# Kernel tuning notes

Measured on AMD Instinct MI355X. Metric: run time of the kernel, lower is better.

Reference implementation:

```python
import jax, jax.numpy as jnp
import numpy as np
import math

B, S, D = 1, 512, 512
N = 8
DH = D // N  # 64


def setup_inputs() -> dict:
    key = jax.random.key(0)
    ks = jax.random.split(key, 12)
    s = 1.0 / math.sqrt(D)
    return {
        "hidden_states": jax.random.normal(ks[0], (B, S, D), dtype=jnp.float32),
        "attention_mask": jnp.ones((B, S), dtype=jnp.float32),
        # Linear weights stored as [in, out] (math-equivalent to torch x @ W.T + b)
        "Wq": jax.random.normal(ks[1], (D, D), dtype=jnp.float32) * s,
        "bq": jax.random.normal(ks[2], (D,), dtype=jnp.float32) * 0.01,
        "Wk": jax.random.normal(ks[3], (D, D), dtype=jnp.float32) * s,
        "bk": jax.random.normal(ks[4], (D,), dtype=jnp.float32) * 0.01,
        "Wv": jax.random.normal(ks[5], (D, D), dtype=jnp.float32) * s,
        "bv": jax.random.normal(ks[6], (D,), dtype=jnp.float32) * 0.01,
        "Wo": jax.random.normal(ks[7], (D, D), dtype=jnp.float32) * s,
        "bo": jax.random.normal(ks[8], (D,), dtype=jnp.float32) * 0.01,
        "gamma": jnp.ones((1,), dtype=jnp.float32) * math.sqrt(DH),
        "alpha": jnp.zeros((1,), dtype=jnp.float32),
    }


def _heads(x):
    # [B,S,D] -> [B,N,S,DH]
    return x.reshape(B, S, N, DH).transpose(0, 2, 1, 3)


def reference(hidden_states, attention_mask, Wq, bq, Wk, bk, Wv, bv, Wo, bo, gamma, alpha):
    q = _heads(hidden_states @ Wq + bq)  # [B,N,S,DH]
    k = _heads(hidden_states @ Wk + bk)
    v = _heads(hidden_states @ Wv + bv)

    # Manhattan-distance scores: z[b,n,i,j] = sum_d |q - k|
    abs_diff = jnp.abs(q[:, :, :, None, :] - k[:, :, None, :, :])  # [B,N,S,S,DH]
    z = abs_diff.sum(-1) / (gamma * math.sqrt(DH))  # [B,N,S,S]
    z_prime = jax.nn.relu(z - alpha)

    # mask: [B,S] -> [B,1,1,S]; masked-out keys get huge inhibition
    z_prime = z_prime + (1.0 - attention_mask)[:, None, None, :] * 1e10

    # inhibition: context[b,n,i,d] = sum_j relu(v[b,n,j,d] - z'[b,n,i,j])
    inhibited = jax.nn.relu(v[:, :, None, :, :] - z_prime[..., None])  # [B,N,S,S,DH]
    context = inhibited.sum(axis=3)  # [B,N,S,DH]  (dropout is identity at eval)

    context = context.transpose(0, 2, 1, 3).reshape(B, S, D)
    return context @ Wo + bo
```

## Files before the change

### kernel.cpp

```cpp
#include <hip/hip_runtime.h>

#define S 512
#define Dm 512

typedef __bf16 bf16x8 __attribute__((ext_vector_type(8)));
typedef float f32x4 __attribute__((ext_vector_type(4)));

template<bool A_BF16, bool TRANSQK>
__global__ __launch_bounds__(256) void gemm_icvt(
    const void* __restrict__ Aptr,
    const float* __restrict__ W0, const float* __restrict__ W1, const float* __restrict__ W2,
    const float* __restrict__ b0, const float* __restrict__ b1, const float* __restrict__ b2,
    float* __restrict__ O0, float* __restrict__ O1, float* __restrict__ O2)
{
    int blk = blockIdx.x;
    int m = blk >> 8;
    int tile = blk & 255;
    const float* W = (m == 0) ? W0 : (m == 1) ? W1 : W2;
    const float* bias = (m == 0) ? b0 : (m == 1) ? b1 : b2;
    float* O = (m == 0) ? O0 : (m == 1) ? O1 : O2;
    int rt = tile >> 4, ct = tile & 15;

    int u = threadIdx.x;
    int w = u >> 6, lane = u & 63;
    int r = lane & 15, kg = lane >> 4;

    int row0 = (rt << 5) + ((w >> 1) << 4);
    int col0 = (ct << 5) + ((w & 1) << 4);

    const float* Bp = W + (kg << 3) * Dm + col0 + r;

    f32x4 acc = {0.f, 0.f, 0.f, 0.f};

    #pragma unroll 4
    for (int k0 = 0; k0 < Dm; k0 += 32) {
        bf16x8 a;
        if constexpr (A_BF16) {
            const __bf16* Ab = (const __bf16*)Aptr;
            a = *(const bf16x8*)(Ab + (row0 + r) * Dm + k0 + (kg << 3));
        } else {
            const float* Af = (const float*)Aptr;
            float4 a0 = *(const float4*)(Af + (row0 + r) * Dm + k0 + (kg << 3));
            float4 a1 = *(const float4*)(Af + (row0 + r) * Dm + k0 + (kg << 3) + 4);
            a[0] = (__bf16)a0.x; a[1] = (__bf16)a0.y; a[2] = (__bf16)a0.z; a[3] = (__bf16)a0.w;
            a[4] = (__bf16)a1.x; a[5] = (__bf16)a1.y; a[6] = (__bf16)a1.z; a[7] = (__bf16)a1.w;
        }
        bf16x8 b;
        #pragma unroll
        for (int t = 0; t < 8; ++t)
            b[t] = (__bf16)Bp[(k0 + t) * Dm];
        acc = __builtin_amdgcn_mfma_f32_16x16x32_bf16(a, b, acc, 0, 0, 0);
    }

    int orow = row0 + (kg << 2);
    float bb = bias[col0 + r];

    if constexpr (TRANSQK) {
        if (m < 2) {
            float4 o = make_float4(acc[0] + bb, acc[1] + bb, acc[2] + bb, acc[3] + bb);
            *(float4*)(O + (col0 + r) * S + orow) = o;
            return;
        }
    }
    #pragma unroll
    for (int t = 0; t < 4; ++t)
        O[(orow + t) * Dm + col0 + r] = acc[t] + bb;
}

__global__ __launch_bounds__(512) void zT_kernel(
    const float* __restrict__ QT, const float* __restrict__ KT,
    const float* __restrict__ mask, const float* __restrict__ gamma,
    const float* __restrict__ alpha,
    float* __restrict__ zp, float* __restrict__ Zpart)
{
    int blk = blockIdx.x;
    int h  = blk >> 6;
    int it = blk & 63;
    int i0 = it << 3;
    int c0 = h << 6;

    int u = threadIdx.x;
    int w = u >> 6, lane = u & 63;
    int jj = (w << 6) + lane;

    const float* kcol = KT + (c0 * S) + jj;
    const float* qrow = QT + (c0 * S) + i0;

    float acc[8] = {};
    #pragma unroll 4
    for (int d = 0; d < 64; ++d) {
        float kv = kcol[d * S];
        float4 qa = *(const float4*)(qrow + d * S);
        float4 qb = *(const float4*)(qrow + d * S + 4);
        acc[0] += fabsf(qa.x - kv);
        acc[1] += fabsf(qa.y - kv);
        acc[2] += fabsf(qa.z - kv);
        acc[3] += fabsf(qa.w - kv);
        acc[4] += fabsf(qb.x - kv);
        acc[5] += fabsf(qb.y - kv);
        acc[6] += fabsf(qb.z - kv);
        acc[7] += fabsf(qb.w - kv);
    }

    float sc = 1.0f / (gamma[0] * 8.0f);
    float al = alpha[0];
    float madd = (1.0f - mask[jj]) * 1e6f;

    float zpv[8];
    #pragma unroll
    for (int r = 0; r < 8; ++r) {
        zpv[r] = fmaxf(acc[r] * sc - al, 0.0f) + madd;
        zp[((h << 9) + i0 + r) * S + jj] = zpv[r];
    }

    #pragma unroll
    for (int r = 0; r < 8; ++r) {
        float v = zpv[r];
        v += __shfl_xor(v, 1, 64);
        v += __shfl_xor(v, 2, 64);
        v += __shfl_xor(v, 4, 64);
        v += __shfl_xor(v, 8, 64);
        v += __shfl_xor(v, 16, 64);
        v += __shfl_xor(v, 32, 64);
        zpv[r] = v;
    }
    if (lane == 0) {
        #pragma unroll
        for (int r = 0; r < 8; ++r)
            Zpart[((h << 9) + i0 + r) * 8 + w] = zpv[r];
    }
}

__global__ __launch_bounds__(512) void ctx_kernel(
    const float* __restrict__ V, const float* __restrict__ zp,
    const float* __restrict__ Zpart, __bf16* __restrict__ ctxb)
{
    int blk = blockIdx.x;
    int h = blk >> 6;
    int it = blk & 63;
    int i0 = it << 3;
    int c0 = h << 6;
    int u = threadIdx.x;
    int w = u >> 6, lane = u & 63;

    __shared__ float part[8][8][64];

    int wu = __builtin_amdgcn_readfirstlane(w);
    float acc[8][4] = {};

    #pragma unroll
    for (int cch = 0; cch < 4; ++cch) {
        int jg = (cch << 7) + (wu << 4);
        float vv[16];
        #pragma unroll
        for (int t = 0; t < 16; ++t)
            vv[t] = V[(jg + t) * Dm + c0 + lane];

        const float* zbase = zp + ((h << 9) + i0) * S + jg;
        #pragma unroll
        for (int ii = 0; ii < 8; ++ii) {
            const float* zrow = zbase + ii * S;
            #pragma unroll
            for (int q4 = 0; q4 < 4; ++q4) {
                float4 z4 = *(const float4*)(zrow + (q4 << 2));
                acc[ii][0] += fmaxf(vv[(q4 << 2) + 0], z4.x);
                acc[ii][1] += fmaxf(vv[(q4 << 2) + 1], z4.y);
                acc[ii][2] += fmaxf(vv[(q4 << 2) + 2], z4.z);
                acc[ii][3] += fmaxf(vv[(q4 << 2) + 3], z4.w);
            }
        }
    }

    #pragma unroll
    for (int ii = 0; ii < 8; ++ii)
        part[w][ii][lane] = (acc[ii][0] + acc[ii][1]) + (acc[ii][2] + acc[ii][3]);
    __syncthreads();
    {
        int ii = u >> 6;
        float s = 0.f;
        #pragma unroll
        for (int ww = 0; ww < 8; ++ww) s += part[ww][ii][lane];
        float zsum = 0.f;
        const float* zpr = Zpart + ((h << 9) + (i0 + ii)) * 8;
        #pragma unroll
        for (int p = 0; p < 8; ++p) zsum += zpr[p];
        ctxb[(i0 + ii) * Dm + c0 + lane] = (__bf16)(s - zsum);
    }
}

extern "C" void kernel_launch(void* const* d_in, const int* in_sizes, int n_in,
                              void* d_out, int out_size, void* d_ws, size_t ws_size,
                              hipStream_t stream) {
    const float* hs    = (const float*)d_in[0];
    const float* mask  = (const float*)d_in[1];
    const float* Wq    = (const float*)d_in[2];
    const float* bq    = (const float*)d_in[3];
    const float* Wk    = (const float*)d_in[4];
    const float* bk    = (const float*)d_in[5];
    const float* Wv    = (const float*)d_in[6];
    const float* bv    = (const float*)d_in[7];
    const float* Wo    = (const float*)d_in[8];
    const float* bo    = (const float*)d_in[9];
    const float* gamma = (const float*)d_in[10];
    const float* alpha = (const float*)d_in[11];
    float* out = (float*)d_out;

    char* base = (char*)d_ws;
    float*  zp    = (float*)(base);
    float*  Zpart = (float*)(base + (8u << 20));
    float*  QT    = (float*)(base + (8u << 20) + (128u << 10));
    float*  KT    = QT + S * Dm;
    float*  Vb    = KT + S * Dm;
    __bf16* Cbf   = (__bf16*)(Vb + S * Dm);

    hipLaunchKernelGGL((gemm_icvt<false, true>), dim3(768), dim3(256), 0, stream,
                       (const void*)hs, Wq, Wk, Wv, bq, bk, bv, QT, KT, Vb);
    hipLaunchKernelGGL(zT_kernel, dim3(512), dim3(512), 0, stream,
                       QT, KT, mask, gamma, alpha, zp, Zpart);
    hipLaunchKernelGGL(ctx_kernel, dim3(512), dim3(512), 0, stream,
                       Vb, zp, Zpart, Cbf);
    hipLaunchKernelGGL((gemm_icvt<true, false>), dim3(256), dim3(256), 0, stream,
                       (const void*)Cbf, Wo, Wo, Wo, bo, bo, bo, out, out, out);
}
```

Measured before the change: 56.83 us.

## Fuse score and context kernels via LDS; pre-transpose weights to bf16

Merges the Manhattan-score kernel and the inhibition-context kernel into one kernel. The 8x512 score tile stays in shared memory instead of going through an 8 MB global buffer, and the row sums are kept in LDS. Adds a prep kernel that converts hidden states to bf16 and transposes all four weight matrices to bf16 [out,in] layout. The GEMMs can then use contiguous 16-byte loads instead of strided scalar fp32 loads. The cost is an extra launch and extra transpose traffic on every call, plus 16 KB+ of LDS per block, which may reduce occupancy in the fused kernel.

Result: faster. 54.19 us (-4.6%).

```diff
diff --git a/kernel.cpp b/kernel.cpp
--- a/kernel.cpp
+++ b/kernel.cpp
@@ -6,17 +6,68 @@
 typedef __bf16 bf16x8 __attribute__((ext_vector_type(8)));
 typedef float f32x4 __attribute__((ext_vector_type(4)));
 
-template<bool A_BF16, bool TRANSQK>
-__global__ __launch_bounds__(256) void gemm_icvt(
-    const void* __restrict__ Aptr,
-    const float* __restrict__ W0, const float* __restrict__ W1, const float* __restrict__ W2,
+__global__ __launch_bounds__(256) void prep_kernel(
+    const float* __restrict__ hs,
+    const float* __restrict__ W0, const float* __restrict__ W1,
+    const float* __restrict__ W2, const float* __restrict__ W3,
+    __bf16* __restrict__ Abf,
+    __bf16* __restrict__ T0, __bf16* __restrict__ T1,
+    __bf16* __restrict__ T2, __bf16* __restrict__ T3)
+{
+    __shared__ __bf16 Tl[64][72];
+    int u = threadIdx.x;
+    if (blockIdx.x < 128) {
+        int i = (blockIdx.x * 256 + u) * 8;
+        float4 x0 = *(const float4*)(hs + i);
+        float4 x1 = *(const float4*)(hs + i + 4);
+        bf16x8 y;
+        y[0] = (__bf16)x0.x; y[1] = (__bf16)x0.y; y[2] = (__bf16)x0.z; y[3] = (__bf16)x0.w;
+        y[4] = (__bf16)x1.x; y[5] = (__bf16)x1.y; y[6] = (__bf16)x1.z; y[7] = (__bf16)x1.w;
+        *(bf16x8*)(Abf + i) = y;
+        return;
+    }
+    int blk = blockIdx.x - 128;
+    int m = blk >> 6;
+    int t = blk & 63;
+    const float* W = (m == 0) ? W0 : (m == 1) ? W1 : (m == 2) ? W2 : W3;
+    __bf16* T = (m == 0) ? T0 : (m == 1) ? T1 : (m == 2) ? T2 : T3;
+    int k0 = (t >> 3) << 6;
+    int n0 = (t & 7) << 6;
+    {
+        int kk = u >> 4;
+        int n4 = (u & 15) << 2;
+        #pragma unroll
+        for (int p = 0; p < 4; ++p) {
+            int k = kk + (p << 4);
+            float4 wv = *(const float4*)(W + (k0 + k) * Dm + n0 + n4);
+            Tl[n4 + 0][k] = (__bf16)wv.x;
+            Tl[n4 + 1][k] = (__bf16)wv.y;
+            Tl[n4 + 2][k] = (__bf16)wv.z;
+            Tl[n4 + 3][k] = (__bf16)wv.w;
+        }
+    }
+    __syncthreads();
+    {
+        int n = u >> 2;
+        int ks = (u & 3) << 4;
+        uint4 d0 = *(const uint4*)&Tl[n][ks];
+        uint4 d1 = *(const uint4*)&Tl[n][ks + 8];
+        *(uint4*)(T + (n0 + n) * Dm + k0 + ks) = d0;
+        *(uint4*)(T + (n0 + n) * Dm + k0 + ks + 8) = d1;
+    }
+}
+
+template<bool TRANSQK>
+__global__ __launch_bounds__(256) void gemm_bf(
+    const __bf16* __restrict__ Abf,
+    const __bf16* __restrict__ T0, const __bf16* __restrict__ T1, const __bf16* __restrict__ T2,
     const float* __restrict__ b0, const float* __restrict__ b1, const float* __restrict__ b2,
     float* __restrict__ O0, float* __restrict__ O1, float* __restrict__ O2)
 {
     int blk = blockIdx.x;
     int m = blk >> 8;
     int tile = blk & 255;
-    const float* W = (m == 0) ? W0 : (m == 1) ? W1 : W2;
+    const __bf16* T = (m == 0) ? T0 : (m == 1) ? T1 : T2;
     const float* bias = (m == 0) ? b0 : (m == 1) ? b1 : b2;
     float* O = (m == 0) ? O0 : (m == 1) ? O1 : O2;
     int rt = tile >> 4, ct = tile & 15;
@@ -28,27 +79,15 @@
     int row0 = (rt << 5) + ((w >> 1) << 4);
     int col0 = (ct << 5) + ((w & 1) << 4);
 
-    const float* Bp = W + (kg << 3) * Dm + col0 + r;
+    const __bf16* Ap = Abf + (row0 + r) * Dm + (kg << 3);
+    const __bf16* Bp = T + (col0 + r) * Dm + (kg << 3);
 
     f32x4 acc = {0.f, 0.f, 0.f, 0.f};
 
     #pragma unroll 4
     for (int k0 = 0; k0 < Dm; k0 += 32) {
-        bf16x8 a;
-        if constexpr (A_BF16) {
-            const __bf16* Ab = (const __bf16*)Aptr;
-            a = *(const bf16x8*)(Ab + (row0 + r) * Dm + k0 + (kg << 3));
-        } else {
-            const float* Af = (const float*)Aptr;
-            float4 a0 = *(const float4*)(Af + (row0 + r) * Dm + k0 + (kg << 3));
-            float4 a1 = *(const float4*)(Af + (row0 + r) * Dm + k0 + (kg << 3) + 4);
-            a[0] = (__bf16)a0.x; a[1] = (__bf16)a0.y; a[2] = (__bf16)a0.z; a[3] = (__bf16)a0.w;
-            a[4] = (__bf16)a1.x; a[5] = (__bf16)a1.y; a[6] = (__bf16)a1.z; a[7] = (__bf16)a1.w;
-        }
-        bf16x8 b;
-        #pragma unroll
-        for (int t = 0; t < 8; ++t)
-            b[t] = (__bf16)Bp[(k0 + t) * Dm];
+        bf16x8 a = *(const bf16x8*)(Ap + k0);
+        bf16x8 b = *(const bf16x8*)(Bp + k0);
         acc = __builtin_amdgcn_mfma_f32_16x16x32_bf16(a, b, acc, 0, 0, 0);
     }
 
@@ -67,11 +106,10 @@
         O[(orow + t) * Dm + col0 + r] = acc[t] + bb;
 }
 
-__global__ __launch_bounds__(512) void zT_kernel(
-    const float* __restrict__ QT, const float* __restrict__ KT,
+__global__ __launch_bounds__(512) void zctx_kernel(
+    const float* __restrict__ QT, const float* __restrict__ KT, const float* __restrict__ V,
     const float* __restrict__ mask, const float* __restrict__ gamma,
-    const float* __restrict__ alpha,
-    float* __restrict__ zp, float* __restrict__ Zpart)
+    const float* __restrict__ alpha, __bf16* __restrict__ ctxb)
 {
     int blk = blockIdx.x;
     int h  = blk >> 6;
@@ -82,6 +120,10 @@
     int u = threadIdx.x;
     int w = u >> 6, lane = u & 63;
     int jj = (w << 6) + lane;
+
+    __shared__ float zs[8][512];
+    __shared__ float zpart[8][8];
+    __shared__ float part[8][8][64];
 
     const float* kcol = KT + (c0 * S) + jj;
     const float* qrow = QT + (c0 * S) + i0;
@@ -110,7 +152,7 @@
     #pragma unroll
     for (int r = 0; r < 8; ++r) {
         zpv[r] = fmaxf(acc[r] * sc - al, 0.0f) + madd;
-        zp[((h << 9) + i0 + r) * S + jj] = zpv[r];
+        zs[r][jj] = zpv[r];
     }
 
     #pragma unroll
@@ -126,27 +168,12 @@
     }
     if (lane == 0) {
         #pragma unroll
-        for (int r = 0; r < 8; ++r)
-            Zpart[((h << 9) + i0 + r) * 8 + w] = zpv[r];
-    }
-}
-
-__global__ __launch_bounds__(512) void ctx_kernel(
-    const float* __restrict__ V, const float* __restrict__ zp,
-    const float* __restrict__ Zpart, __bf16* __restrict__ ctxb)
-{
-    int blk = blockIdx.x;
-    int h = blk >> 6;
-    int it = blk & 63;
-    int i0 = it << 3;
-    int c0 = h << 6;
-    int u = threadIdx.x;
-    int w = u >> 6, lane = u & 63;
-
-    __shared__ float part[8][8][64];
+        for (int r = 0; r < 8; ++r) zpart[w][r] = zpv[r];
+    }
+    __syncthreads();
 
     int wu = __builtin_amdgcn_readfirstlane(w);
-    float acc[8][4] = {};
+    float a2[8][4] = {};
 
     #pragma unroll
     for (int cch = 0; cch < 4; ++cch) {
@@ -156,34 +183,32 @@
         for (int t = 0; t < 16; ++t)
             vv[t] = V[(jg + t) * Dm + c0 + lane];
 
-        const float* zbase = zp + ((h << 9) + i0) * S + jg;
         #pragma unroll
         for (int ii = 0; ii < 8; ++ii) {
-            const float* zrow = zbase + ii * S;
             #pragma unroll
             for (int q4 = 0; q4 < 4; ++q4) {
-                float4 z4 = *(const float4*)(zrow + (q4 << 2));
-                acc[ii][0] += fmaxf(vv[(q4 << 2) + 0], z4.x);
-                acc[ii][1] += fmaxf(vv[(q4 << 2) + 1], z4.y);
-                acc[ii][2] += fmaxf(vv[(q4 << 2) + 2], z4.z);
-                acc[ii][3] += fmaxf(vv[(q4 << 2) + 3], z4.w);
+                float4 z4 = *(const float4*)&zs[ii][jg + (q4 << 2)];
+                a2[ii][0] += fmaxf(vv[(q4 << 2) + 0], z4.x);
+                a2[ii][1] += fmaxf(vv[(q4 << 2) + 1], z4.y);
+                a2[ii][2] += fmaxf(vv[(q4 << 2) + 2], z4.z);
+                a2[ii][3] += fmaxf(vv[(q4 << 2) + 3], z4.w);
             }
         }
     }
 
     #pragma unroll
     for (int ii = 0; ii < 8; ++ii)
-        part[w][ii][lane] = (acc[ii][0] + acc[ii][1]) + (acc[ii][2] + acc[ii][3]);
+        part[w][ii][lane] = (a2[ii][0] + a2[ii][1]) + (a2[ii][2] + a2[ii][3]);
     __syncthreads();
+
     {
         int ii = u >> 6;
         float s = 0.f;
         #pragma unroll
         for (int ww = 0; ww < 8; ++ww) s += part[ww][ii][lane];
         float zsum = 0.f;
-        const float* zpr = Zpart + ((h << 9) + (i0 + ii)) * 8;
-        #pragma unroll
-        for (int p = 0; p < 8; ++p) zsum += zpr[p];
+        #pragma unroll
+        for (int p = 0; p < 8; ++p) zsum += zpart[p][ii];
         ctxb[(i0 + ii) * Dm + c0 + lane] = (__bf16)(s - zsum);
     }
 }
@@ -206,19 +231,22 @@
     float* out = (float*)d_out;
 
     char* base = (char*)d_ws;
-    float*  zp    = (float*)(base);
-    float*  Zpart = (float*)(base + (8u << 20));
-    float*  QT    = (float*)(base + (8u << 20) + (128u << 10));
-    float*  KT    = QT + S * Dm;
-    float*  Vb    = KT + S * Dm;
-    __bf16* Cbf   = (__bf16*)(Vb + S * Dm);
-
-    hipLaunchKernelGGL((gemm_icvt<false, true>), dim3(768), dim3(256), 0, stream,
-                       (const void*)hs, Wq, Wk, Wv, bq, bk, bv, QT, KT, Vb);
-    hipLaunchKernelGGL(zT_kernel, dim3(512), dim3(512), 0, stream,
-                       QT, KT, mask, gamma, alpha, zp, Zpart);
-    hipLaunchKernelGGL(ctx_kernel, dim3(512), dim3(512), 0, stream,
-                       Vb, zp, Zpart, Cbf);
-    hipLaunchKernelGGL((gemm_icvt<true, false>), dim3(256), dim3(256), 0, stream,
-                       (const void*)Cbf, Wo, Wo, Wo, bo, bo, bo, out, out, out);
-}
+    float*  QT  = (float*)(base);
+    float*  KT  = QT + S * Dm;
+    float*  Vb  = KT + S * Dm;
+    __bf16* Abf = (__bf16*)(Vb + S * Dm);
+    __bf16* T0  = Abf + S * Dm;
+    __bf16* T1  = T0 + S * Dm;
+    __bf16* T2  = T1 + S * Dm;
+    __bf16* T3  = T2 + S * Dm;
+    __bf16* Cbf = T3 + S * Dm;
+
+    hipLaunchKernelGGL(prep_kernel, dim3(384), dim3(256), 0, stream,
+                       hs, Wq, Wk, Wv, Wo, Abf, T0, T1, T2, T3);
+    hipLaunchKernelGGL((gemm_bf<true>), dim3(768), dim3(256), 0, stream,
+                       Abf, T0, T1, T2, bq, bk, bv, QT, KT, Vb);
+    hipLaunchKernelGGL(zctx_kernel, dim3(512), dim3(512), 0, stream,
+                       QT, KT, Vb, mask, gamma, alpha, Cbf);
+    hipLaunchKernelGGL((gemm_bf<false>), dim3(256), dim3(256), 0, stream,
+                       Cbf, T3, T3, T3, bo, bo, bo, out, out, out);
+}
```

## Fuse score and context kernels via LDS; stage weight tiles through shared memory

Applied to the files above, without the earlier changes.

The Manhattan-score kernel and the inhibition-context kernel are merged. The 8x512 z' tile and the per-row partial sums now stay in LDS, so the 8 MB zp buffer no longer round-trips through global memory and one launch is dropped. The GEMM also stages the weight tile through LDS with coalesced float4 loads and a transposed bf16 layout, replacing strided per-element global loads. In exchange, both kernels use more LDS and extra barriers, which may lower occupancy.

Measured after the change: 56.01 us. About the same (-1.4%).

```diff
diff --git a/kernel.cpp b/kernel.cpp
--- a/kernel.cpp
+++ b/kernel.cpp
@@ -7,7 +7,7 @@
 typedef float f32x4 __attribute__((ext_vector_type(4)));
 
 template<bool A_BF16, bool TRANSQK>
-__global__ __launch_bounds__(256) void gemm_icvt(
+__global__ __launch_bounds__(256) void gemm_stage(
     const void* __restrict__ Aptr,
     const float* __restrict__ W0, const float* __restrict__ W1, const float* __restrict__ W2,
     const float* __restrict__ b0, const float* __restrict__ b1, const float* __restrict__ b2,
@@ -26,30 +26,50 @@
     int r = lane & 15, kg = lane >> 4;
 
     int row0 = (rt << 5) + ((w >> 1) << 4);
-    int col0 = (ct << 5) + ((w & 1) << 4);
-
-    const float* Bp = W + (kg << 3) * Dm + col0 + r;
+    int colb = ct << 5;
+    int col0 = colb + ((w & 1) << 4);
+
+    __shared__ __bf16 Tl[32][72];
 
     f32x4 acc = {0.f, 0.f, 0.f, 0.f};
 
-    #pragma unroll 4
-    for (int k0 = 0; k0 < Dm; k0 += 32) {
-        bf16x8 a;
-        if constexpr (A_BF16) {
-            const __bf16* Ab = (const __bf16*)Aptr;
-            a = *(const bf16x8*)(Ab + (row0 + r) * Dm + k0 + (kg << 3));
-        } else {
-            const float* Af = (const float*)Aptr;
-            float4 a0 = *(const float4*)(Af + (row0 + r) * Dm + k0 + (kg << 3));
-            float4 a1 = *(const float4*)(Af + (row0 + r) * Dm + k0 + (kg << 3) + 4);
-            a[0] = (__bf16)a0.x; a[1] = (__bf16)a0.y; a[2] = (__bf16)a0.z; a[3] = (__bf16)a0.w;
-            a[4] = (__bf16)a1.x; a[5] = (__bf16)a1.y; a[6] = (__bf16)a1.z; a[7] = (__bf16)a1.w;
-        }
-        bf16x8 b;
-        #pragma unroll
-        for (int t = 0; t < 8; ++t)
-            b[t] = (__bf16)Bp[(k0 + t) * Dm];
-        acc = __builtin_amdgcn_mfma_f32_16x16x32_bf16(a, b, acc, 0, 0, 0);
+    int skk = u >> 2;
+    int sn4 = (u & 3) << 3;
+
+    for (int k0 = 0; k0 < Dm; k0 += 64) {
+        {
+            const float* wp = W + (k0 + skk) * Dm + colb + sn4;
+            float4 w0v = *(const float4*)(wp);
+            float4 w1v = *(const float4*)(wp + 4);
+            Tl[sn4 + 0][skk] = (__bf16)w0v.x;
+            Tl[sn4 + 1][skk] = (__bf16)w0v.y;
+            Tl[sn4 + 2][skk] = (__bf16)w0v.z;
+            Tl[sn4 + 3][skk] = (__bf16)w0v.w;
+            Tl[sn4 + 4][skk] = (__bf16)w1v.x;
+            Tl[sn4 + 5][skk] = (__bf16)w1v.y;
+            Tl[sn4 + 6][skk] = (__bf16)w1v.z;
+            Tl[sn4 + 7][skk] = (__bf16)w1v.w;
+        }
+        __syncthreads();
+
+        #pragma unroll
+        for (int s = 0; s < 2; ++s) {
+            int ks = k0 + (s << 5);
+            bf16x8 a;
+            if constexpr (A_BF16) {
+                const __bf16* Ab = (const __bf16*)Aptr;
+                a = *(const bf16x8*)(Ab + (row0 + r) * Dm + ks + (kg << 3));
+            } else {
+                const float* Af = (const float*)Aptr;
+                float4 a0 = *(const float4*)(Af + (row0 + r) * Dm + ks + (kg << 3));
+                float4 a1 = *(const float4*)(Af + (row0 + r) * Dm + ks + (kg << 3) + 4);
+                a[0] = (__bf16)a0.x; a[1] = (__bf16)a0.y; a[2] = (__bf16)a0.z; a[3] = (__bf16)a0.w;
+                a[4] = (__bf16)a1.x; a[5] = (__bf16)a1.y; a[6] = (__bf16)a1.z; a[7] = (__bf16)a1.w;
+            }
+            bf16x8 b = *(const bf16x8*)&Tl[((w & 1) << 4) + r][(s << 5) + (kg << 3)];
+            acc = __builtin_amdgcn_mfma_f32_16x16x32_bf16(a, b, acc, 0, 0, 0);
+        }
+        __syncthreads();
     }
 
     int orow = row0 + (kg << 2);
@@ -67,11 +87,10 @@
         O[(orow + t) * Dm + col0 + r] = acc[t] + bb;
 }
 
-__global__ __launch_bounds__(512) void zT_kernel(
-    const float* __restrict__ QT, const float* __restrict__ KT,
+__global__ __launch_bounds__(512) void zctx_kernel(
+    const float* __restrict__ QT, const float* __restrict__ KT, const float* __restrict__ V,
     const float* __restrict__ mask, const float* __restrict__ gamma,
-    const float* __restrict__ alpha,
-    float* __restrict__ zp, float* __restrict__ Zpart)
+    const float* __restrict__ alpha, __bf16* __restrict__ ctxb)
 {
     int blk = blockIdx.x;
     int h  = blk >> 6;
@@ -82,6 +101,10 @@
     int u = threadIdx.x;
     int w = u >> 6, lane = u & 63;
     int jj = (w << 6) + lane;
+
+    __shared__ float zs[8][512];
+    __shared__ float zpart[8][8];
+    __shared__ float part[8][8][64];
 
     const float* kcol = KT + (c0 * S) + jj;
     const float* qrow = QT + (c0 * S) + i0;
@@ -110,7 +133,7 @@
     #pragma unroll
     for (int r = 0; r < 8; ++r) {
         zpv[r] = fmaxf(acc[r] * sc - al, 0.0f) + madd;
-        zp[((h << 9) + i0 + r) * S + jj] = zpv[r];
+        zs[r][jj] = zpv[r];
     }
 
     #pragma unroll
@@ -126,27 +149,12 @@
     }
     if (lane == 0) {
         #pragma unroll
-        for (int r = 0; r < 8; ++r)
-            Zpart[((h << 9) + i0 + r) * 8 + w] = zpv[r];
-    }
-}
-
-__global__ __launch_bounds__(512) void ctx_kernel(
-    const float* __restrict__ V, const float* __restrict__ zp,
-    const float* __restrict__ Zpart, __bf16* __restrict__ ctxb)
-{
-    int blk = blockIdx.x;
-    int h = blk >> 6;
-    int it = blk & 63;
-    int i0 = it << 3;
-    int c0 = h << 6;
-    int u = threadIdx.x;
-    int w = u >> 6, lane = u & 63;
-
-    __shared__ float part[8][8][64];
+        for (int r = 0; r < 8; ++r) zpart[w][r] = zpv[r];
+    }
+    __syncthreads();
 
     int wu = __builtin_amdgcn_readfirstlane(w);
-    float acc[8][4] = {};
+    float a2[8][4] = {};
 
     #pragma unroll
     for (int cch = 0; cch < 4; ++cch) {
@@ -156,34 +164,32 @@
         for (int t = 0; t < 16; ++t)
             vv[t] = V[(jg + t) * Dm + c0 + lane];
 
-        const float* zbase = zp + ((h << 9) + i0) * S + jg;
         #pragma unroll
         for (int ii = 0; ii < 8; ++ii) {
-            const float* zrow = zbase + ii * S;
             #pragma unroll
             for (int q4 = 0; q4 < 4; ++q4) {
-                float4 z4 = *(const float4*)(zrow + (q4 << 2));
-                acc[ii][0] += fmaxf(vv[(q4 << 2) + 0], z4.x);
-                acc[ii][1] += fmaxf(vv[(q4 << 2) + 1], z4.y);
-                acc[ii][2] += fmaxf(vv[(q4 << 2) + 2], z4.z);
-                acc[ii][3] += fmaxf(vv[(q4 << 2) + 3], z4.w);
+                float4 z4 = *(const float4*)&zs[ii][jg + (q4 << 2)];
+                a2[ii][0] += fmaxf(vv[(q4 << 2) + 0], z4.x);
+                a2[ii][1] += fmaxf(vv[(q4 << 2) + 1], z4.y);
+                a2[ii][2] += fmaxf(vv[(q4 << 2) + 2], z4.z);
+                a2[ii][3] += fmaxf(vv[(q4 << 2) + 3], z4.w);
             }
         }
     }
 
     #pragma unroll
     for (int ii = 0; ii < 8; ++ii)
-        part[w][ii][lane] = (acc[ii][0] + acc[ii][1]) + (acc[ii][2] + acc[ii][3]);
+        part[w][ii][lane] = (a2[ii][0] + a2[ii][1]) + (a2[ii][2] + a2[ii][3]);
     __syncthreads();
+
     {
         int ii = u >> 6;
         float s = 0.f;
         #pragma unroll
         for (int ww = 0; ww < 8; ++ww) s += part[ww][ii][lane];
         float zsum = 0.f;
-        const float* zpr = Zpart + ((h << 9) + (i0 + ii)) * 8;
-        #pragma unroll
-        for (int p = 0; p < 8; ++p) zsum += zpr[p];
+        #pragma unroll
+        for (int p = 0; p < 8; ++p) zsum += zpart[p][ii];
         ctxb[(i0 + ii) * Dm + c0 + lane] = (__bf16)(s - zsum);
     }
 }
@@ -206,19 +212,15 @@
     float* out = (float*)d_out;
 
     char* base = (char*)d_ws;
-    float*  zp    = (float*)(base);
-    float*  Zpart = (float*)(base + (8u << 20));
-    float*  QT    = (float*)(base + (8u << 20) + (128u << 10));
-    float*  KT    = QT + S * Dm;
-    float*  Vb    = KT + S * Dm;
-    __bf16* Cbf   = (__bf16*)(Vb + S * Dm);
-
-    hipLaunchKernelGGL((gemm_icvt<false, true>), dim3(768), dim3(256), 0, stream,
+    float*  QT  = (float*)(base);
+    float*  KT  = QT + S * Dm;
+    float*  Vb  = KT + S * Dm;
+    __bf16* Cbf = (__bf16*)(Vb + S * Dm);
+
+    hipLaunchKernelGGL((gemm_stage<false, true>), dim3(768), dim3(256), 0, stream,
                        (const void*)hs, Wq, Wk, Wv, bq, bk, bv, QT, KT, Vb);
-    hipLaunchKernelGGL(zT_kernel, dim3(512), dim3(512), 0, stream,
-                       QT, KT, mask, gamma, alpha, zp, Zpart);
-    hipLaunchKernelGGL(ctx_kernel, dim3(512), dim3(512), 0, stream,
-                       Vb, zp, Zpart, Cbf);
-    hipLaunchKernelGGL((gemm_icvt<true, false>), dim3(256), dim3(256), 0, stream,
+    hipLaunchKernelGGL(zctx_kernel, dim3(512), dim3(512), 0, stream,
+                       QT, KT, Vb, mask, gamma, alpha, Cbf);
+    hipLaunchKernelGGL((gemm_stage<true, false>), dim3(256), dim3(256), 0, stream,
                        (const void*)Cbf, Wo, Wo, Wo, bo, bo, bo, out, out, out);
 }
```
